# Performance work log

Measured on AMD Instinct MI355X. Metric: run time of the kernel, lower is better.

Reference implementation:

```python
import jax, jax.numpy as jnp
import numpy as np

N_ATOMS = 100_000  # number of center atoms
K = 16             # neighbors per atom within cutoff (uniform for static shapes)


def setup_inputs() -> dict:
    # pair_i: sorted center-atom index per neighbor pair, K neighbors per atom.
    pair_i = jnp.repeat(jnp.arange(N_ATOMS, dtype=jnp.int32), K)  # [N_ATOMS*K]
    return {"pair_i": pair_i, "n_atoms": N_ATOMS, "max_neighbors": K}


def reference(pair_i, n_atoms, max_neighbors):
    """Segmented combinations: for each atom's contiguous neighbor block,
    emit all unique (j,k) pair-index combinations, exactly matching the
    torch.combinations lexicographic order of the original Python loop.
    Assumes uniform neighbor count == max_neighbors (as built in setup)."""
    ones = jnp.ones_like(pair_i)
    counts = jax.ops.segment_sum(ones, pair_i, num_segments=n_atoms)  # [n_atoms]
    starts = jnp.cumsum(counts) - counts                              # block offsets (prefix sum)

    # within-block combination template, shared by all atoms
    pu, pv = jnp.triu_indices(max_neighbors, k=1)  # [T_per], T_per = K*(K-1)/2
    t_per = pu.shape[0]

    idx_i = jnp.repeat(jnp.arange(n_atoms, dtype=pair_i.dtype), t_per)          # [n_atoms*T_per]
    idx_j = (starts[:, None] + pu[None, :]).reshape(-1).astype(pair_i.dtype)    # [n_atoms*T_per]
    idx_k = (starts[:, None] + pv[None, :]).reshape(-1).astype(pair_i.dtype)    # [n_atoms*T_per]
    return idx_i, idx_j, idx_k
```

## Files before the change

### kernel.cpp

```cpp
#include <hip/hip_runtime.h>


constexpr int K      = 16;
constexpr int T_PER  = K * (K - 1) / 2;
constexpr int GROUPS = T_PER / 4;

struct Tbl { unsigned u[GROUPS]; unsigned v[GROUPS]; };
constexpr Tbl make_tbl() {
    Tbl t{};
    int idx = 0;
    for (int a = 0; a < K; ++a)
        for (int b = a + 1; b < K; ++b) {
            t.u[idx / 4] |= (unsigned)a << ((idx % 4) * 8);
            t.v[idx / 4] |= (unsigned)b << ((idx % 4) * 8);
            ++idx;
        }
    return t;
}
__device__ constexpr Tbl TBL = make_tbl();

__global__ void starts_kernel(const int* __restrict__ pair_i, int* __restrict__ starts,
                              int n_atoms, int m) {
    int a = blockIdx.x * blockDim.x + threadIdx.x;
    if (a >= n_atoms) return;
    int lo = 0, hi = m;
    while (lo < hi) {
        int mid = (lo + hi) >> 1;
        if (pair_i[mid] < a) lo = mid + 1; else hi = mid;
    }
    starts[a] = lo;
}

__global__ void gen_kernel(const int* __restrict__ starts, int* __restrict__ out,
                           int per_arr_groups) {
    int g = blockIdx.x * blockDim.x + threadIdx.x;
    if (g >= per_arr_groups) return;
    int atom = g / GROUPS;
    int r    = g - atom * GROUPS;

    int start = starts ? starts[atom] : atom * K;

    unsigned ub = TBL.u[r];
    unsigned vb = TBL.v[r];

    int4* o = (int4*)out;
    o[g] = make_int4(atom, atom, atom, atom);
    o[g + per_arr_groups] = make_int4(start + (int)(ub & 0xff),
                                      start + (int)((ub >> 8)  & 0xff),
                                      start + (int)((ub >> 16) & 0xff),
                                      start + (int)((ub >> 24) & 0xff));
    o[g + 2 * per_arr_groups] = make_int4(start + (int)(vb & 0xff),
                                          start + (int)((vb >> 8)  & 0xff),
                                          start + (int)((vb >> 16) & 0xff),
                                          start + (int)((vb >> 24) & 0xff));
}

extern "C" void kernel_launch(void* const* d_in, const int* in_sizes, int n_in,
                              void* d_out, int out_size, void* d_ws, size_t ws_size,
                              hipStream_t stream) {
    const int* pair_i = (const int*)d_in[0];
    const int  m      = in_sizes[0];
    const int  n_atoms = m / K;

    int* out = (int*)d_out;
    const int per_arr_groups = n_atoms * GROUPS;

    int* starts = nullptr;
    if (ws_size >= (size_t)n_atoms * sizeof(int)) {
        starts = (int*)d_ws;
        const int b1 = 256;
        starts_kernel<<<(n_atoms + b1 - 1) / b1, b1, 0, stream>>>(pair_i, starts, n_atoms, m);
    }

    const int b2 = 256;
    gen_kernel<<<(per_arr_groups + b2 - 1) / b2, b2, 0, stream>>>(starts, out, per_arr_groups);
}
```

Measured before the change: 156.9 us.

## Fuse block-start search into generator kernel with shared starts and nontemporal stores

Merges the binary-search starts kernel and the combination generator into one kernel: each block handles 32 atoms, computes their block starts into shared memory, then 960 threads write the index triples. This removes a kernel launch and the workspace round-trip for starts. Output writes use nontemporal stores to avoid polluting caches on the large streaming write. The trade-off is that only 32 threads do the binary search while the rest wait at the barrier, and the large 960-thread blocks may limit occupancy.

Measured after the change: 193.2 us. 23.1% more time.

```diff
diff --git a/kernel.cpp b/kernel.cpp
--- a/kernel.cpp
+++ b/kernel.cpp
@@ -1,9 +1,13 @@
 #include <hip/hip_runtime.h>
 
 
-constexpr int K      = 16;
-constexpr int T_PER  = K * (K - 1) / 2;
-constexpr int GROUPS = T_PER / 4;
+constexpr int K       = 16;
+constexpr int T_PER   = K * (K - 1) / 2;
+constexpr int GROUPS  = T_PER / 4;
+constexpr int APB     = 32;
+constexpr int THREADS = APB * GROUPS;
+
+typedef int iv4 __attribute__((ext_vector_type(4)));
 
 struct Tbl { unsigned u[GROUPS]; unsigned v[GROUPS]; };
 constexpr Tbl make_tbl() {
@@ -19,59 +23,66 @@
 }
 __device__ constexpr Tbl TBL = make_tbl();
 
-__global__ void starts_kernel(const int* __restrict__ pair_i, int* __restrict__ starts,
-                              int n_atoms, int m) {
-    int a = blockIdx.x * blockDim.x + threadIdx.x;
-    if (a >= n_atoms) return;
-    int lo = 0, hi = m;
-    while (lo < hi) {
-        int mid = (lo + hi) >> 1;
-        if (pair_i[mid] < a) lo = mid + 1; else hi = mid;
+__global__ __launch_bounds__(THREADS, 2)
+void triple_gen_fused(const int* __restrict__ pair_i, int* __restrict__ out,
+                      int n_atoms, int m, int per_arr_groups) {
+    __shared__ int s_start[APB];
+
+    const int t  = threadIdx.x;
+    const int a0 = blockIdx.x * APB;
+
+    if (t < APB) {
+        int a = a0 + t;
+        int lo = 0;
+        if (a < n_atoms) {
+            int hi = m;
+            while (lo < hi) {
+                int mid = (lo + hi) >> 1;
+                if (pair_i[mid] < a) lo = mid + 1; else hi = mid;
+            }
+        }
+        s_start[t] = lo;
     }
-    starts[a] = lo;
-}
+    __syncthreads();
 
-__global__ void gen_kernel(const int* __restrict__ starts, int* __restrict__ out,
-                           int per_arr_groups) {
-    int g = blockIdx.x * blockDim.x + threadIdx.x;
-    if (g >= per_arr_groups) return;
-    int atom = g / GROUPS;
-    int r    = g - atom * GROUPS;
+    const int local_atom = t / GROUPS;
+    const int r          = t - local_atom * GROUPS;
+    const int atom       = a0 + local_atom;
+    if (atom >= n_atoms) return;
 
-    int start = starts ? starts[atom] : atom * K;
+    const int start = s_start[local_atom];
+    const unsigned ub = TBL.u[r];
+    const unsigned vb = TBL.v[r];
 
-    unsigned ub = TBL.u[r];
-    unsigned vb = TBL.v[r];
+    const int g = atom * GROUPS + r;
+    iv4* o = (iv4*)out;
 
-    int4* o = (int4*)out;
-    o[g] = make_int4(atom, atom, atom, atom);
-    o[g + per_arr_groups] = make_int4(start + (int)(ub & 0xff),
-                                      start + (int)((ub >> 8)  & 0xff),
-                                      start + (int)((ub >> 16) & 0xff),
-                                      start + (int)((ub >> 24) & 0xff));
-    o[g + 2 * per_arr_groups] = make_int4(start + (int)(vb & 0xff),
-                                          start + (int)((vb >> 8)  & 0xff),
-                                          start + (int)((vb >> 16) & 0xff),
-                                          start + (int)((vb >> 24) & 0xff));
+    iv4 vi; vi[0] = atom; vi[1] = atom; vi[2] = atom; vi[3] = atom;
+    iv4 vj; vj[0] = start + (int)(ub & 0xff);
+            vj[1] = start + (int)((ub >> 8)  & 0xff);
+            vj[2] = start + (int)((ub >> 16) & 0xff);
+            vj[3] = start + (int)((ub >> 24) & 0xff);
+    iv4 vk; vk[0] = start + (int)(vb & 0xff);
+            vk[1] = start + (int)((vb >> 8)  & 0xff);
+            vk[2] = start + (int)((vb >> 16) & 0xff);
+            vk[3] = start + (int)((vb >> 24) & 0xff);
+
+    __builtin_nontemporal_store(vi, &o[g]);
+    __builtin_nontemporal_store(vj, &o[g + per_arr_groups]);
+    __builtin_nontemporal_store(vk, &o[g + 2 * per_arr_groups]);
 }
 
 extern "C" void kernel_launch(void* const* d_in, const int* in_sizes, int n_in,
                               void* d_out, int out_size, void* d_ws, size_t ws_size,
                               hipStream_t stream) {
-    const int* pair_i = (const int*)d_in[0];
-    const int  m      = in_sizes[0];
+    const int* pair_i  = (const int*)d_in[0];
+    const int  m       = in_sizes[0];
     const int  n_atoms = m / K;
 
     int* out = (int*)d_out;
     const int per_arr_groups = n_atoms * GROUPS;
+    const int n_blocks = (n_atoms + APB - 1) / APB;
 
-    int* starts = nullptr;
-    if (ws_size >= (size_t)n_atoms * sizeof(int)) {
-        starts = (int*)d_ws;
-        const int b1 = 256;
-        starts_kernel<<<(n_atoms + b1 - 1) / b1, b1, 0, stream>>>(pair_i, starts, n_atoms, m);
-    }
-
-    const int b2 = 256;
-    gen_kernel<<<(per_arr_groups + b2 - 1) / b2, b2, 0, stream>>>(starts, out, per_arr_groups);
+    triple_gen_fused<<<n_blocks, THREADS, 0, stream>>>(pair_i, out, n_atoms, m,
+                                                       per_arr_groups);
 }
```
